# Kernel optimization log

Hardware: AMD Instinct MI355X
Metric: run time of the kernel (lower is better)

## Reference

```python
import jax, jax.numpy as jnp
import numpy as np

B, C, H, W = 4, 16, 320, 640


def _propagate_front(x, g):
    """Linear propagation along leading axis.
    x, g: [L, ...]. out[0] = x[0]; out[i] = x[i]*(1-g[i]) + g[i]*out[i-1].
    """
    def step(prev, xg):
        xr, gr = xg
        out = xr * (1.0 - gr) + gr * prev
        return out, out
    _, ys = jax.lax.scan(step, x[0], (x[1:], g[1:]))
    return jnp.concatenate([x[:1], ys], axis=0)


def _propagate(x, g, axis, reverse):
    xm = jnp.moveaxis(x, axis, 0)
    gm = jnp.moveaxis(g, axis, 0)
    if reverse:
        xm = xm[::-1]
        gm = gm[::-1]
    ym = _propagate_front(xm, gm)
    if reverse:
        ym = ym[::-1]
    return jnp.moveaxis(ym, 0, axis)


def setup_inputs() -> dict:
    key = jax.random.key(0)
    ks = jax.random.split(key, 5)
    shape = (B, C, H, W)
    return {
        "input": jax.random.normal(ks[0], shape, dtype=jnp.float32),
        "g0": jax.random.uniform(ks[1], shape, dtype=jnp.float32),
        "g1": jax.random.uniform(ks[2], shape, dtype=jnp.float32),
        "g2": jax.random.uniform(ks[3], shape, dtype=jnp.float32),
        "g3": jax.random.uniform(ks[4], shape, dtype=jnp.float32),
    }


def reference(input, g0, g1, g2, g3):
    # 4-directional gated recurrent grid propagation, fused by elementwise max.
    r_down = _propagate(input, g0, axis=2, reverse=False)   # top -> bottom over H
    r_up = _propagate(input, g1, axis=2, reverse=True)      # bottom -> top over H
    r_right = _propagate(input, g2, axis=3, reverse=False)  # left -> right over W
    r_left = _propagate(input, g3, axis=3, reverse=True)    # right -> left over W
    return jnp.maximum(jnp.maximum(jnp.maximum(r_down, r_up), r_right), r_left)
```

## Files before the change

### kernel.cpp

```cpp
#include <hip/hip_runtime.h>

constexpr int Bn = 4;
constexpr int Cn = 16;
constexpr int Hn = 320;
constexpr int Wn = 640;
constexpr int NCOL = Bn * Cn * Wn;
constexpr int NROW = Bn * Cn * Hn;

constexpr int HSEG = 32;
constexpr int NSEG = Hn / HSEG;
constexpr int VBLK = NSEG * 64;

__global__ __launch_bounds__(VBLK) void vert(
    const float* __restrict__ x, const float* __restrict__ g0,
    const float* __restrict__ g1, float* __restrict__ outDown,
    float* __restrict__ outUp) {
  __shared__ float As[NSEG][64], Bs[NSEG][64], Cs[NSEG][64];
  constexpr int NGRP = NCOL / 64;
  int blk = blockIdx.x;
  bool bwd = blk >= NGRP;
  int grp = bwd ? blk - NGRP : blk;
  int bc = grp / (Wn / 64);
  int w0 = (grp % (Wn / 64)) * 64;
  int s = threadIdx.x >> 6;
  int l = threadIdx.x & 63;
  size_t colbase = (size_t)bc * (Hn * Wn) + w0 + l;
  const float* __restrict__ gp = bwd ? g1 : g0;
  float* __restrict__ op = bwd ? outUp : outDown;

  float y[HSEG], P[HSEG];
  float yy = 0.0f, pp = 1.0f;
#pragma unroll
  for (int i = 0; i < HSEG; ++i) {
    int r = bwd ? (Hn - 1 - (s * HSEG + i)) : (s * HSEG + i);
    size_t off = colbase + (size_t)r * Wn;
    float xv = x[off];
    float gv = gp[off];
    float b = (s == 0 && i == 0) ? 0.0f : gv;
    yy = fmaf(b, yy - xv, xv);
    pp *= b;
    y[i] = yy;
    P[i] = pp;
  }
  As[s][l] = yy;
  Bs[s][l] = pp;
  __syncthreads();
  if (threadIdx.x < 64) {
    float c = 0.0f;
#pragma unroll
    for (int ss = 0; ss < NSEG; ++ss) {
      Cs[ss][l] = c;
      c = fmaf(Bs[ss][l], c, As[ss][l]);
    }
  }
  __syncthreads();
  float c = Cs[s][l];
#pragma unroll
  for (int i = 0; i < HSEG; ++i) {
    int r = bwd ? (Hn - 1 - (s * HSEG + i)) : (s * HSEG + i);
    op[colbase + (size_t)r * Wn] = fmaf(P[i], c, y[i]);
  }
}

__global__ __launch_bounds__(256) void vert_fused(
    const float* __restrict__ x, const float* __restrict__ g0,
    const float* __restrict__ g1, float* __restrict__ out) {
  int col = blockIdx.x * 256 + threadIdx.x;
  int w = col % Wn;
  int bc = col / Wn;
  size_t base = (size_t)bc * Hn * Wn + w;
  const float* xp = x + base;
  float* op = out + base;
  {
    const float* gp = g0 + base;
    float y = xp[0];
    op[0] = y;
#pragma unroll 8
    for (int h = 1; h < Hn; ++h) {
      float xv = xp[(size_t)h * Wn];
      float gv = gp[(size_t)h * Wn];
      y = fmaf(gv, y - xv, xv);
      op[(size_t)h * Wn] = y;
    }
  }
  {
    const float* gp = g1 + base;
    float y = xp[(size_t)(Hn - 1) * Wn];
    op[(size_t)(Hn - 1) * Wn] = fmaxf(op[(size_t)(Hn - 1) * Wn], y);
#pragma unroll 8
    for (int h = Hn - 2; h >= 0; --h) {
      float xv = xp[(size_t)h * Wn];
      float gv = gp[(size_t)h * Wn];
      y = fmaf(gv, y - xv, xv);
      op[(size_t)h * Wn] = fmaxf(op[(size_t)h * Wn], y);
    }
  }
}

constexpr int WSEG = 16;
constexpr int NLANE = Wn / WSEG;

template <bool HAS_UP>
__global__ __launch_bounds__(512) void horiz(
    const float* __restrict__ x, const float* __restrict__ g2,
    const float* __restrict__ g3, const float* __restrict__ down,
    const float* __restrict__ up, float* __restrict__ out) {
  int wv = threadIdx.x >> 6;
  int l = threadIdx.x & 63;
  int row = blockIdx.x * 8 + wv;
  bool act = l < NLANE;
  size_t base = (size_t)row * Wn + (size_t)l * WSEG;

  float xv[WSEG], gv[WSEG], rr[WSEG], rl[WSEG], P[WSEG];

  if (act) {
#pragma unroll
    for (int q = 0; q < WSEG / 4; ++q) {
      float4 t = ((const float4*)(x + base))[q];
      xv[4 * q] = t.x; xv[4 * q + 1] = t.y; xv[4 * q + 2] = t.z; xv[4 * q + 3] = t.w;
      float4 u = ((const float4*)(g2 + base))[q];
      gv[4 * q] = u.x; gv[4 * q + 1] = u.y; gv[4 * q + 2] = u.z; gv[4 * q + 3] = u.w;
    }
  }

  float yy = 0.0f, pp = 1.0f;
#pragma unroll
  for (int i = 0; i < WSEG; ++i) {
    float b = (l == 0 && i == 0) ? 0.0f : gv[i];
    yy = fmaf(b, yy - xv[i], xv[i]);
    pp *= b;
    rr[i] = yy;
    P[i] = pp;
  }
  float A = act ? yy : 0.0f;
  float B = act ? pp : 1.0f;
#pragma unroll
  for (int off = 1; off < 64; off <<= 1) {
    float Au = __shfl_up(A, off);
    float Bu = __shfl_up(B, off);
    if (l >= off) { A = fmaf(B, Au, A); B *= Bu; }
  }
  float c = __shfl_up(A, 1);
  if (l == 0) c = 0.0f;
#pragma unroll
  for (int i = 0; i < WSEG; ++i) rr[i] = fmaf(P[i], c, rr[i]);

  if (act) {
#pragma unroll
    for (int q = 0; q < WSEG / 4; ++q) {
      float4 u = ((const float4*)(g3 + base))[q];
      gv[4 * q] = u.x; gv[4 * q + 1] = u.y; gv[4 * q + 2] = u.z; gv[4 * q + 3] = u.w;
    }
  }
  yy = 0.0f; pp = 1.0f;
#pragma unroll
  for (int i = WSEG - 1; i >= 0; --i) {
    float b = (l == NLANE - 1 && i == WSEG - 1) ? 0.0f : gv[i];
    yy = fmaf(b, yy - xv[i], xv[i]);
    pp *= b;
    rl[i] = yy;
    P[i] = pp;
  }
  A = act ? yy : 0.0f;
  B = act ? pp : 1.0f;
#pragma unroll
  for (int off = 1; off < 64; off <<= 1) {
    float Ad = __shfl_down(A, off);
    float Bd = __shfl_down(B, off);
    if (l + off < 64) { A = fmaf(B, Ad, A); B *= Bd; }
  }
  float c2 = __shfl_down(A, 1);
  if (l >= NLANE - 1) c2 = 0.0f;
#pragma unroll
  for (int i = 0; i < WSEG; ++i) rl[i] = fmaf(P[i], c2, rl[i]);

  if (act) {
#pragma unroll
    for (int q = 0; q < WSEG / 4; ++q) {
      float4 dn = ((const float4*)(down + base))[q];
      float4 uv;
      if (HAS_UP) uv = ((const float4*)(up + base))[q];
      float4 o;
      o.x = fmaxf(fmaxf(dn.x, rr[4 * q + 0]), rl[4 * q + 0]);
      o.y = fmaxf(fmaxf(dn.y, rr[4 * q + 1]), rl[4 * q + 1]);
      o.z = fmaxf(fmaxf(dn.z, rr[4 * q + 2]), rl[4 * q + 2]);
      o.w = fmaxf(fmaxf(dn.w, rr[4 * q + 3]), rl[4 * q + 3]);
      if (HAS_UP) {
        o.x = fmaxf(o.x, uv.x);
        o.y = fmaxf(o.y, uv.y);
        o.z = fmaxf(o.z, uv.z);
        o.w = fmaxf(o.w, uv.w);
      }
      ((float4*)(out + base))[q] = o;
    }
  }
}

extern "C" void kernel_launch(void* const* d_in, const int* in_sizes, int n_in,
                              void* d_out, int out_size, void* d_ws,
                              size_t ws_size, hipStream_t stream) {
  const float* x = (const float*)d_in[0];
  const float* g0 = (const float*)d_in[1];
  const float* g1 = (const float*)d_in[2];
  const float* g2 = (const float*)d_in[3];
  const float* g3 = (const float*)d_in[4];
  float* out = (float*)d_out;

  size_t need = (size_t)out_size * sizeof(float);
  if (ws_size >= need) {
    float* ws = (float*)d_ws;
    vert<<<2 * (NCOL / 64), VBLK, 0, stream>>>(x, g0, g1, out, ws);
    horiz<true><<<NROW / 8, 512, 0, stream>>>(x, g2, g3, out, ws, out);
  } else {
    vert_fused<<<NCOL / 256, 256, 0, stream>>>(x, g0, g1, out);
    horiz<false><<<NROW / 8, 512, 0, stream>>>(x, g2, g3, out, nullptr, out);
  }
}
```

Before: 290.2 us.

## Recompute vertical scans instead of holding registers; stage horizontal rows in LDS

The vertical kernel now does both directions in one block. It drops the per-element y/P register arrays and re-reads x and the gates in a second pass to produce the outputs, which cuts register pressure so the occupancy hint of 6 can apply, at the cost of re-reading inputs. The horizontal kernel now loads four rows into shared memory with coalesced float4 loads. All 64 lanes are active, with 10 elements each, and the scan results are written back to LDS before a coalesced max-combine and store. This trades the extra global re-reads and LDS traffic for better occupancy and coalescing.

```diff
diff --git a/kernel.cpp b/kernel.cpp
--- a/kernel.cpp
+++ b/kernel.cpp
@@ -11,54 +11,87 @@
 constexpr int NSEG = Hn / HSEG;
 constexpr int VBLK = NSEG * 64;
 
-__global__ __launch_bounds__(VBLK) void vert(
+__global__ __launch_bounds__(VBLK, 6) void vert2(
     const float* __restrict__ x, const float* __restrict__ g0,
-    const float* __restrict__ g1, float* __restrict__ outDown,
-    float* __restrict__ outUp) {
-  __shared__ float As[NSEG][64], Bs[NSEG][64], Cs[NSEG][64];
-  constexpr int NGRP = NCOL / 64;
-  int blk = blockIdx.x;
-  bool bwd = blk >= NGRP;
-  int grp = bwd ? blk - NGRP : blk;
+    const float* __restrict__ g1, float* __restrict__ outD,
+    float* __restrict__ outU) {
+  __shared__ float A0[NSEG][64], B0[NSEG][64], A1[NSEG][64], B1[NSEG][64];
+  int grp = blockIdx.x;
   int bc = grp / (Wn / 64);
   int w0 = (grp % (Wn / 64)) * 64;
   int s = threadIdx.x >> 6;
   int l = threadIdx.x & 63;
   size_t colbase = (size_t)bc * (Hn * Wn) + w0 + l;
-  const float* __restrict__ gp = bwd ? g1 : g0;
-  float* __restrict__ op = bwd ? outUp : outDown;
-
-  float y[HSEG], P[HSEG];
-  float yy = 0.0f, pp = 1.0f;
-#pragma unroll
-  for (int i = 0; i < HSEG; ++i) {
-    int r = bwd ? (Hn - 1 - (s * HSEG + i)) : (s * HSEG + i);
-    size_t off = colbase + (size_t)r * Wn;
-    float xv = x[off];
-    float gv = gp[off];
-    float b = (s == 0 && i == 0) ? 0.0f : gv;
-    yy = fmaf(b, yy - xv, xv);
-    pp *= b;
-    y[i] = yy;
-    P[i] = pp;
-  }
-  As[s][l] = yy;
-  Bs[s][l] = pp;
-  __syncthreads();
-  if (threadIdx.x < 64) {
+
+  {
+    size_t off = colbase + (size_t)(s * HSEG) * Wn;
+    float a = 0.0f, b = 1.0f;
+#pragma unroll
+    for (int i = 0; i < HSEG; ++i) {
+      float xv = x[off];
+      float gv = g0[off];
+      float bb = (s == 0 && i == 0) ? 0.0f : gv;
+      a = fmaf(bb, a - xv, xv);
+      b *= bb;
+      off += Wn;
+    }
+    A0[s][l] = a; B0[s][l] = b;
+  }
+  {
+    size_t off = colbase + (size_t)(Hn - 1 - s * HSEG) * Wn;
+    float a = 0.0f, b = 1.0f;
+#pragma unroll
+    for (int i = 0; i < HSEG; ++i) {
+      float xv = x[off];
+      float gv = g1[off];
+      float bb = (s == 0 && i == 0) ? 0.0f : gv;
+      a = fmaf(bb, a - xv, xv);
+      b *= bb;
+      off -= Wn;
+    }
+    A1[s][l] = a; B1[s][l] = b;
+  }
+  __syncthreads();
+
+  if (threadIdx.x < 128) {
+    bool d1 = threadIdx.x >= 64;
+    int ll = threadIdx.x & 63;
     float c = 0.0f;
 #pragma unroll
     for (int ss = 0; ss < NSEG; ++ss) {
-      Cs[ss][l] = c;
-      c = fmaf(Bs[ss][l], c, As[ss][l]);
-    }
-  }
-  __syncthreads();
-  float c = Cs[s][l];
-#pragma unroll
-  for (int i = 0; i < HSEG; ++i) {
-    int r = bwd ? (Hn - 1 - (s * HSEG + i)) : (s * HSEG + i);
-    op[colbase + (size_t)r * Wn] = fmaf(P[i], c, y[i]);
+      float a = d1 ? A1[ss][ll] : A0[ss][ll];
+      float b = d1 ? B1[ss][ll] : B0[ss][ll];
+      if (d1) A1[ss][ll] = c; else A0[ss][ll] = c;
+      c = fmaf(b, c, a);
+    }
+  }
+  __syncthreads();
+
+  {
+    float y = A0[s][l];
+    size_t off = colbase + (size_t)(s * HSEG) * Wn;
+#pragma unroll
+    for (int i = 0; i < HSEG; ++i) {
+      float xv = x[off];
+      float gv = g0[off];
+      float bb = (s == 0 && i == 0) ? 0.0f : gv;
+      y = fmaf(bb, y - xv, xv);
+      outD[off] = y;
+      off += Wn;
+    }
+  }
+  {
+    float y = A1[s][l];
+    size_t off = colbase + (size_t)(Hn - 1 - s * HSEG) * Wn;
+#pragma unroll
+    for (int i = 0; i < HSEG; ++i) {
+      float xv = x[off];
+      float gv = g1[off];
+      float bb = (s == 0 && i == 0) ? 0.0f : gv;
+      y = fmaf(bb, y - xv, xv);
+      outU[off] = y;
+      off -= Wn;
+    }
   }
 }
 
@@ -97,102 +130,104 @@
   }
 }
 
-constexpr int WSEG = 16;
-constexpr int NLANE = Wn / WSEG;
+constexpr int WSEG = 10;
 
 template <bool HAS_UP>
-__global__ __launch_bounds__(512) void horiz(
+__global__ __launch_bounds__(256) void horiz3(
     const float* __restrict__ x, const float* __restrict__ g2,
     const float* __restrict__ g3, const float* __restrict__ down,
     const float* __restrict__ up, float* __restrict__ out) {
-  int wv = threadIdx.x >> 6;
-  int l = threadIdx.x & 63;
-  int row = blockIdx.x * 8 + wv;
-  bool act = l < NLANE;
-  size_t base = (size_t)row * Wn + (size_t)l * WSEG;
-
-  float xv[WSEG], gv[WSEG], rr[WSEG], rl[WSEG], P[WSEG];
-
-  if (act) {
-#pragma unroll
-    for (int q = 0; q < WSEG / 4; ++q) {
-      float4 t = ((const float4*)(x + base))[q];
-      xv[4 * q] = t.x; xv[4 * q + 1] = t.y; xv[4 * q + 2] = t.z; xv[4 * q + 3] = t.w;
-      float4 u = ((const float4*)(g2 + base))[q];
-      gv[4 * q] = u.x; gv[4 * q + 1] = u.y; gv[4 * q + 2] = u.z; gv[4 * q + 3] = u.w;
-    }
-  }
-
-  float yy = 0.0f, pp = 1.0f;
-#pragma unroll
-  for (int i = 0; i < WSEG; ++i) {
-    float b = (l == 0 && i == 0) ? 0.0f : gv[i];
-    yy = fmaf(b, yy - xv[i], xv[i]);
-    pp *= b;
-    rr[i] = yy;
-    P[i] = pp;
-  }
-  float A = act ? yy : 0.0f;
-  float B = act ? pp : 1.0f;
-#pragma unroll
-  for (int off = 1; off < 64; off <<= 1) {
-    float Au = __shfl_up(A, off);
-    float Bu = __shfl_up(B, off);
-    if (l >= off) { A = fmaf(B, Au, A); B *= Bu; }
-  }
-  float c = __shfl_up(A, 1);
-  if (l == 0) c = 0.0f;
-#pragma unroll
-  for (int i = 0; i < WSEG; ++i) rr[i] = fmaf(P[i], c, rr[i]);
-
-  if (act) {
-#pragma unroll
-    for (int q = 0; q < WSEG / 4; ++q) {
-      float4 u = ((const float4*)(g3 + base))[q];
-      gv[4 * q] = u.x; gv[4 * q + 1] = u.y; gv[4 * q + 2] = u.z; gv[4 * q + 3] = u.w;
-    }
-  }
-  yy = 0.0f; pp = 1.0f;
-#pragma unroll
-  for (int i = WSEG - 1; i >= 0; --i) {
-    float b = (l == NLANE - 1 && i == WSEG - 1) ? 0.0f : gv[i];
-    yy = fmaf(b, yy - xv[i], xv[i]);
-    pp *= b;
-    rl[i] = yy;
-    P[i] = pp;
-  }
-  A = act ? yy : 0.0f;
-  B = act ? pp : 1.0f;
-#pragma unroll
-  for (int off = 1; off < 64; off <<= 1) {
-    float Ad = __shfl_down(A, off);
-    float Bd = __shfl_down(B, off);
-    if (l + off < 64) { A = fmaf(B, Ad, A); B *= Bd; }
-  }
-  float c2 = __shfl_down(A, 1);
-  if (l >= NLANE - 1) c2 = 0.0f;
-#pragma unroll
-  for (int i = 0; i < WSEG; ++i) rl[i] = fmaf(P[i], c2, rl[i]);
-
-  if (act) {
-#pragma unroll
-    for (int q = 0; q < WSEG / 4; ++q) {
-      float4 dn = ((const float4*)(down + base))[q];
-      float4 uv;
-      if (HAS_UP) uv = ((const float4*)(up + base))[q];
-      float4 o;
-      o.x = fmaxf(fmaxf(dn.x, rr[4 * q + 0]), rl[4 * q + 0]);
-      o.y = fmaxf(fmaxf(dn.y, rr[4 * q + 1]), rl[4 * q + 1]);
-      o.z = fmaxf(fmaxf(dn.z, rr[4 * q + 2]), rl[4 * q + 2]);
-      o.w = fmaxf(fmaxf(dn.w, rr[4 * q + 3]), rl[4 * q + 3]);
-      if (HAS_UP) {
-        o.x = fmaxf(o.x, uv.x);
-        o.y = fmaxf(o.y, uv.y);
-        o.z = fmaxf(o.z, uv.z);
-        o.w = fmaxf(o.w, uv.w);
-      }
-      ((float4*)(out + base))[q] = o;
-    }
+  __shared__ float xs[4 * Wn], rrs[4 * Wn], rls[4 * Wn];
+  const int tid = threadIdx.x, wv = tid >> 6, l = tid & 63;
+  const size_t rowbase = (size_t)blockIdx.x * 4 * Wn;
+
+  const float4* xg = (const float4*)(x + rowbase);
+  const float4* g2g = (const float4*)(g2 + rowbase);
+  const float4* g3g = (const float4*)(g3 + rowbase);
+  float4* xsv = (float4*)xs;
+  float4* rrv = (float4*)rrs;
+  float4* rlv = (float4*)rls;
+#pragma unroll
+  for (int i = tid; i < Wn; i += 256) {
+    xsv[i] = xg[i];
+    rrv[i] = g2g[i];
+    rlv[i] = g3g[i];
+  }
+  __syncthreads();
+
+  const int rb = wv * Wn + l * WSEG;
+  float xl[WSEG], gl[WSEG], yl[WSEG], pl[WSEG];
+#pragma unroll
+  for (int i = 0; i < WSEG; ++i) { xl[i] = xs[rb + i]; gl[i] = rrs[rb + i]; }
+
+  {
+    float y = 0.0f, p = 1.0f;
+#pragma unroll
+    for (int i = 0; i < WSEG; ++i) {
+      float bb = (l == 0 && i == 0) ? 0.0f : gl[i];
+      y = fmaf(bb, y - xl[i], xl[i]);
+      p *= bb;
+      yl[i] = y; pl[i] = p;
+    }
+    float A = y, B = p;
+#pragma unroll
+    for (int off = 1; off < 64; off <<= 1) {
+      float Au = __shfl_up(A, off);
+      float Bu = __shfl_up(B, off);
+      if (l >= off) { A = fmaf(B, Au, A); B *= Bu; }
+    }
+    float c = __shfl_up(A, 1);
+    if (l == 0) c = 0.0f;
+#pragma unroll
+    for (int i = 0; i < WSEG; ++i) rrs[rb + i] = fmaf(pl[i], c, yl[i]);
+  }
+
+#pragma unroll
+  for (int i = 0; i < WSEG; ++i) gl[i] = rls[rb + i];
+  {
+    float y = 0.0f, p = 1.0f;
+#pragma unroll
+    for (int i = WSEG - 1; i >= 0; --i) {
+      float bb = (l == 63 && i == WSEG - 1) ? 0.0f : gl[i];
+      y = fmaf(bb, y - xl[i], xl[i]);
+      p *= bb;
+      yl[i] = y; pl[i] = p;
+    }
+    float A = y, B = p;
+#pragma unroll
+    for (int off = 1; off < 64; off <<= 1) {
+      float Ad = __shfl_down(A, off);
+      float Bd = __shfl_down(B, off);
+      if (l + off < 64) { A = fmaf(B, Ad, A); B *= Bd; }
+    }
+    float c = __shfl_down(A, 1);
+    if (l == 63) c = 0.0f;
+#pragma unroll
+    for (int i = 0; i < WSEG; ++i) rls[rb + i] = fmaf(pl[i], c, yl[i]);
+  }
+  __syncthreads();
+
+  const float4* dn4 = (const float4*)(down + rowbase);
+  const float4* up4 = (const float4*)(up + rowbase);
+  float4* o4 = (float4*)(out + rowbase);
+#pragma unroll
+  for (int i = tid; i < Wn; i += 256) {
+    float4 a = rrv[i];
+    float4 b = rlv[i];
+    float4 d = dn4[i];
+    float4 o;
+    o.x = fmaxf(fmaxf(a.x, b.x), d.x);
+    o.y = fmaxf(fmaxf(a.y, b.y), d.y);
+    o.z = fmaxf(fmaxf(a.z, b.z), d.z);
+    o.w = fmaxf(fmaxf(a.w, b.w), d.w);
+    if (HAS_UP) {
+      float4 u = up4[i];
+      o.x = fmaxf(o.x, u.x);
+      o.y = fmaxf(o.y, u.y);
+      o.z = fmaxf(o.z, u.z);
+      o.w = fmaxf(o.w, u.w);
+    }
+    o4[i] = o;
   }
 }
 
@@ -209,10 +244,10 @@
   size_t need = (size_t)out_size * sizeof(float);
   if (ws_size >= need) {
     float* ws = (float*)d_ws;
-    vert<<<2 * (NCOL / 64), VBLK, 0, stream>>>(x, g0, g1, out, ws);
-    horiz<true><<<NROW / 8, 512, 0, stream>>>(x, g2, g3, out, ws, out);
+    vert2<<<NCOL / 64, VBLK, 0, stream>>>(x, g0, g1, out, ws);
+    horiz3<true><<<NROW / 4, 256, 0, stream>>>(x, g2, g3, out, ws, out);
   } else {
     vert_fused<<<NCOL / 256, 256, 0, stream>>>(x, g0, g1, out);
-    horiz<false><<<NROW / 8, 512, 0, stream>>>(x, g2, g3, out, nullptr, out);
-  }
-}
+    horiz3<false><<<NROW / 4, 256, 0, stream>>>(x, g2, g3, out, nullptr, out);
+  }
+}
```

Result: slower. 470.7 us (+62.2%).
